# Performance work log

Measured on AMD Instinct MI355X. Metric: run time of the kernel, lower is better.

## Reference

```python
import jax, jax.numpy as jnp
import numpy as np

G, L, NSTA, NSRC, K = 10000, 1000, 400, 2000, 15
SIG = 10.0
FTRNS_SCALE = 1000.0  # ftrns1_diff(x) = x * 1000 (km -> m style linear transform)
FUDGE = 1.0


def setup_inputs() -> dict:
    key = jax.random.key(0)
    ks = jax.random.split(key, 9)
    sta = 10.0 * jax.random.normal(ks[0], (NSTA, 3), jnp.float32)
    src = 10.0 * jax.random.normal(ks[1], (NSRC, 3), jnp.float32)
    mag = jax.random.normal(ks[2], (NSRC,), jnp.float32)
    phase = jax.random.randint(ks[3], (NSTA,), 0, 2)
    x_grid = 10.0 * jax.random.normal(ks[4], (G, 3), jnp.float32)
    locs_ref = 10.0 * jax.random.normal(ks[5], (L, 3), jnp.float32)
    mag_coef = jnp.ones(2, jnp.float32)
    epicenter_spatial_coef = jnp.ones(2, jnp.float32)
    depth_spatial_coef = 0.1 * jax.random.normal(ks[6], (2,), jnp.float32)
    coefs = 0.1 * jax.random.normal(ks[7], (G, L, 2), jnp.float32)
    coefs_ker = SIG + 0.1 * jax.random.normal(ks[8], (G, L, 3), jnp.float32)
    return {"sta": sta, "src": src, "mag": mag, "phase": phase,
            "x_grid": x_grid, "locs_ref": locs_ref, "mag_coef": mag_coef,
            "epicenter_spatial_coef": epicenter_spatial_coef,
            "depth_spatial_coef": depth_spatial_coef,
            "coefs": coefs, "coefs_ker": coefs_ker}


def _ftrns(x):
    return x * FTRNS_SCALE


def _magnitude_fwd(sta, src, mag, phase, x_grid, locs_ref, mag_coef,
                   epicenter_spatial_coef, depth_spatial_coef, coefs, coefs_ker):
    sp = jax.nn.softplus
    zvec = jnp.array([1.0, 1.0, 0.0], dtype=sta.dtype)

    # nearest reference station index for each station (knn k=1)
    locs_ref_cart = _ftrns(locs_ref) / 1000.0            # [L,3]
    sta_pos = _ftrns(sta) / 1000.0                       # [Nsta,3]
    d2_ref = ((sta_pos[:, None, :] - locs_ref_cart[None, :, :]) ** 2).sum(-1)
    sta_ind = jnp.argmin(d2_ref, axis=1)                 # [Nsta]

    # pairwise log-distance matrices [Nsrc, Nsta]
    pw_log_dist_zero = jnp.log10(
        jnp.linalg.norm(_ftrns(src * zvec)[:, None, :] - _ftrns(sta * zvec)[None, :, :], axis=2) + FUDGE)
    pw_log_dist_depths = jnp.log10(jnp.abs(src[:, 2][:, None] - sta[:, 2][None, :]) + FUDGE)

    # --- anisotropic kNN interpolation of coefs[:, sta_ind, :] from grid to src ---
    pos1 = _ftrns(x_grid) / 1000.0                       # [G,3]
    pos2 = _ftrns(src) / 1000.0                          # [Nsrc,3]
    dq = ((pos2[:, None, :] - pos1[None, :, :]) ** 2).sum(-1)  # [Nsrc,G]
    _, idx = jax.lax.top_k(-dq, K)                       # [Nsrc,K] nearest grid nodes

    coefs_sub = coefs[:, sta_ind, :]                     # [G,Nsta,2]
    ker_sub = coefs_ker[:, sta_ind, :]                   # [G,Nsta,3]

    diff = pos1[idx] - pos2[:, None, :]                  # [Nsrc,K,3]
    ker_e = sp(ker_sub[idx])                             # [Nsrc,K,Nsta,3]
    w = jnp.exp(-0.5 * ((diff[:, :, None, :] / ker_e) ** 2).sum(-1))  # [Nsrc,K,Nsta]
    wsum = w.sum(axis=1, keepdims=True)                  # [Nsrc,1,Nsta]
    wsum = jnp.where(wsum == 0.0, 1.0, wsum)
    w = w / wsum
    bias_l = jnp.einsum('qkn,qknc->qnc', w, coefs_sub[idx])  # [Nsrc,Nsta,2]

    # phase-selected bias and coefficients
    bias = jnp.where(phase[None, :] == 0, bias_l[:, :, 0], bias_l[:, :, 1])  # [Nsrc,Nsta]
    mc = sp(mag_coef)[phase]                             # [Nsta]
    ec = sp(epicenter_spatial_coef)[phase]
    dc = depth_spatial_coef[phase]

    log_amp = (mag[:, None] * mc[None, :]
               - ec[None, :] * pw_log_dist_zero
               + dc[None, :] * pw_log_dist_depths
               + bias)                                   # [Nsrc,Nsta]
    return log_amp


def reference(sta, src, mag, phase, x_grid, locs_ref, mag_coef,
              epicenter_spatial_coef, depth_spatial_coef, coefs, coefs_ker):
    return _magnitude_fwd(sta, src, mag, phase, x_grid, locs_ref, mag_coef,
                          epicenter_spatial_coef, depth_spatial_coef, coefs, coefs_ker)
```

## Files before the change

kernel.cpp:

```cpp
#include <hip/hip_runtime.h>
#include <hip/hip_fp16.h>
#include <cstddef>

#define G_N   10000
#define L_N   1000
#define NSTA  400
#define NSRC  2000
#define KK    15
#define NBIN  2048
#define CAP   512

__device__ __forceinline__ float tr1k(float x) {
    return (x * 1000.0f) / 1000.0f;
}

__device__ __forceinline__ float softplus(float x) {
    return fmaxf(x, 0.0f) + log1pf(expf(-fabsf(x)));
}

__device__ __forceinline__ float softplus_fast(float x) {
    return fmaxf(x, 0.0f) + __logf(1.0f + __expf(-fabsf(x)));
}

__device__ __forceinline__ bool lexless(float v1, int i1, float v2, int i2) {
    return (v1 < v2) || (v1 == v2 && i1 < i2);
}

__global__ void sta_ind_kernel(const float* __restrict__ sta,
                               const float* __restrict__ locs_ref,
                               int* __restrict__ sta_ind,
                               int* __restrict__ used) {
#pragma clang fp contract(off)
    const int i    = blockIdx.x;
    const int lane = threadIdx.x;

    if (used) {
        int z = blockIdx.x * 64 + lane;
        if (z < G_N) used[z] = 0;
    }

    const float sx = tr1k(sta[i * 3 + 0]);
    const float sy = tr1k(sta[i * 3 + 1]);
    const float sz = tr1k(sta[i * 3 + 2]);
    float best = INFINITY;
    int   bidx = 0x7fffffff;
    for (int j = lane; j < L_N; j += 64) {
        float dx = sx - tr1k(locs_ref[j * 3 + 0]);
        float dy = sy - tr1k(locs_ref[j * 3 + 1]);
        float dz = sz - tr1k(locs_ref[j * 3 + 2]);
        float d  = (dx * dx + dy * dy) + dz * dz;
        if (lexless(d, j, best, bidx)) { best = d; bidx = j; }
    }
    for (int off = 1; off < 64; off <<= 1) {
        float ov = __shfl_xor(best, off);
        int   oi = __shfl_xor(bidx, off);
        if (lexless(ov, oi, best, bidx)) { best = ov; bidx = oi; }
    }
    if (lane == 0) sta_ind[i] = bidx;
}

__global__ __launch_bounds__(256, 8) void topk_kernel(const float* __restrict__ src,
                                                      const float* __restrict__ x_grid,
                                                      int* __restrict__ idx_out,
                                                      int* __restrict__ used) {
#pragma clang fp contract(off)
    const int s    = blockIdx.x;
    const int tid  = threadIdx.x;
    const int lane = tid & 63;
    const int wv   = tid >> 6;

    __shared__ unsigned int s_hist[NBIN];
    __shared__ int          s_cand[CAP];
    __shared__ float        s_cd[CAP];
    __shared__ int          s_cnt;
    __shared__ int          s_binB;
    __shared__ int          s_nle;
    __shared__ float        s_mv[4];
    __shared__ int          s_mi[4];
    __shared__ int          s_ch[KK];

    for (int b = tid; b < NBIN; b += 256) s_hist[b] = 0u;
    if (tid == 0) s_cnt = 0;
    __syncthreads();

    const float sx = tr1k(src[s * 3 + 0]);
    const float sy = tr1k(src[s * 3 + 1]);
    const float sz = tr1k(src[s * 3 + 2]);

    for (int g = tid; g < G_N; g += 256) {
        float dx = sx - tr1k(x_grid[g * 3 + 0]);
        float dy = sy - tr1k(x_grid[g * 3 + 1]);
        float dz = sz - tr1k(x_grid[g * 3 + 2]);
        float d  = (dx * dx + dy * dy) + dz * dz;
        atomicAdd(&s_hist[__float_as_uint(d) >> 20], 1u);
    }
    __syncthreads();

    if (wv == 0) {
        const int chunk = NBIN / 64;
        const int base  = lane * chunk;
        unsigned int cs = 0;
        for (int b = 0; b < chunk; ++b) cs += s_hist[base + b];
        unsigned int pfx = cs;
        for (int off = 1; off < 64; off <<= 1) {
            unsigned int o = __shfl_up(pfx, off);
            if (lane >= off) pfx += o;
        }
        unsigned long long m = __ballot(pfx >= (unsigned)KK);
        int fl = __ffsll((unsigned long long)m) - 1;
        if (lane == fl) {
            unsigned int acc = pfx - cs;
            int b = base;
            for (;;) {
                acc += s_hist[b];
                if (acc >= (unsigned)KK) break;
                ++b;
            }
            s_binB = b;
            s_nle  = (int)acc;
        }
    }
    __syncthreads();

    const int binB = s_binB;
    const int nle  = s_nle;

    if (nle <= CAP) {
        for (int g = tid; g < G_N; g += 256) {
            float dx = sx - tr1k(x_grid[g * 3 + 0]);
            float dy = sy - tr1k(x_grid[g * 3 + 1]);
            float dz = sz - tr1k(x_grid[g * 3 + 2]);
            float d  = (dx * dx + dy * dy) + dz * dz;
            if ((int)(__float_as_uint(d) >> 20) <= binB) {
                int p = atomicAdd(&s_cnt, 1);
                s_cand[p] = g;
                s_cd[p]   = d;
            }
        }
        __syncthreads();
        if (wv == 0) {
            const int n = s_cnt;
            float vals[KK];
            int   ids[KK];
#pragma unroll
            for (int j = 0; j < KK; ++j) { vals[j] = INFINITY; ids[j] = 0x7fffffff; }
            for (int c = lane; c < n; c += 64) {
                int   g = s_cand[c];
                float d = s_cd[c];
                if (lexless(d, g, vals[KK - 1], ids[KK - 1])) {
                    float cv = d; int ci = g;
#pragma unroll
                    for (int j = 0; j < KK; ++j) {
                        bool sw = lexless(cv, ci, vals[j], ids[j]);
                        float tv = sw ? vals[j] : cv;
                        int   ti = sw ? ids[j]  : ci;
                        vals[j]  = sw ? cv : vals[j];
                        ids[j]   = sw ? ci : ids[j];
                        cv = tv; ci = ti;
                    }
                }
            }
            for (int r = 0; r < KK; ++r) {
                float v  = vals[0];
                int   id = ids[0];
                int   who = lane;
                for (int off = 1; off < 64; off <<= 1) {
                    float ov = __shfl_xor(v, off);
                    int   oi = __shfl_xor(id, off);
                    int   ow = __shfl_xor(who, off);
                    if (lexless(ov, oi, v, id)) { v = ov; id = oi; who = ow; }
                }
                if (lane == 0) {
                    idx_out[s * KK + r] = id;
                    if (used) used[id] = 1;
                }
                if (who == lane) {
#pragma unroll
                    for (int j = 0; j < KK - 1; ++j) { vals[j] = vals[j + 1]; ids[j] = ids[j + 1]; }
                    vals[KK - 1] = INFINITY;
                    ids[KK - 1]  = 0x7fffffff;
                }
            }
        }
    } else {
        for (int r = 0; r < KK; ++r) {
            float v  = INFINITY;
            int   id = 0x7fffffff;
            for (int g = tid; g < G_N; g += 256) {
                bool skip = false;
                for (int j = 0; j < r; ++j) skip = skip || (s_ch[j] == g);
                if (skip) continue;
                float dx = sx - tr1k(x_grid[g * 3 + 0]);
                float dy = sy - tr1k(x_grid[g * 3 + 1]);
                float dz = sz - tr1k(x_grid[g * 3 + 2]);
                float d  = (dx * dx + dy * dy) + dz * dz;
                if (lexless(d, g, v, id)) { v = d; id = g; }
            }
            for (int off = 1; off < 64; off <<= 1) {
                float ov = __shfl_xor(v, off);
                int   oi = __shfl_xor(id, off);
                if (lexless(ov, oi, v, id)) { v = ov; id = oi; }
            }
            if (lane == 0) { s_mv[wv] = v; s_mi[wv] = id; }
            __syncthreads();
            if (tid == 0) {
                float bv = s_mv[0]; int bi = s_mi[0];
                for (int w = 1; w < 4; ++w)
                    if (lexless(s_mv[w], s_mi[w], bv, bi)) { bv = s_mv[w]; bi = s_mi[w]; }
                s_ch[r] = bi;
                idx_out[s * KK + r] = bi;
                if (used) used[bi] = 1;
            }
            __syncthreads();
        }
    }
}

__global__ __launch_bounds__(256) void pack_kernel(
    const float* __restrict__ coefs, const float* __restrict__ coefs_ker,
    const int* __restrict__ sta_ind, const int* __restrict__ phase,
    const int* __restrict__ used,
    uint2* __restrict__ pk)
{
    const int g = blockIdx.x;
    if (!used[g]) return;
    const int tid = threadIdx.x;

    __shared__ float s_ker[L_N * 3];
    __shared__ float s_c[L_N * 2];

    const float4* kr4 = (const float4*)(coefs_ker + (size_t)g * (L_N * 3));
    const float4* cr4 = (const float4*)(coefs     + (size_t)g * (L_N * 2));
    float4* sk4 = (float4*)s_ker;
    float4* sc4 = (float4*)s_c;
#pragma unroll
    for (int j = 0; j < 3; ++j) {
        int p = tid + j * 256;
        if (p < (L_N * 3) / 4) sk4[p] = kr4[p];
    }
#pragma unroll
    for (int j = 0; j < 2; ++j) {
        int p = tid + j * 256;
        if (p < (L_N * 2) / 4) sc4[p] = cr4[p];
    }
    const int i1 = tid + 256;
    const int st0 = sta_ind[tid];
    const int ph0 = phase[tid];
    const int st1 = (i1 < NSTA) ? sta_ind[i1] : 0;
    const int ph1 = (i1 < NSTA) ? phase[i1] : 0;
    __syncthreads();

    {
        float rk0 = 1.0f / softplus_fast(s_ker[st0 * 3 + 0]);
        float rk1 = 1.0f / softplus_fast(s_ker[st0 * 3 + 1]);
        float rk2 = 1.0f / softplus_fast(s_ker[st0 * 3 + 2]);
        float c   = (ph0 == 0) ? s_c[st0 * 2 + 0] : s_c[st0 * 2 + 1];
        __half2 a = __floats2half2_rn(rk0, rk1);
        __half2 b = __floats2half2_rn(rk2, c);
        uint2 u;
        u.x = *reinterpret_cast<unsigned int*>(&a);
        u.y = *reinterpret_cast<unsigned int*>(&b);
        pk[(size_t)g * NSTA + tid] = u;
    }
    if (i1 < NSTA) {
        float rk0 = 1.0f / softplus_fast(s_ker[st1 * 3 + 0]);
        float rk1 = 1.0f / softplus_fast(s_ker[st1 * 3 + 1]);
        float rk2 = 1.0f / softplus_fast(s_ker[st1 * 3 + 2]);
        float c   = (ph1 == 0) ? s_c[st1 * 2 + 0] : s_c[st1 * 2 + 1];
        __half2 a = __floats2half2_rn(rk0, rk1);
        __half2 b = __floats2half2_rn(rk2, c);
        uint2 u;
        u.x = *reinterpret_cast<unsigned int*>(&a);
        u.y = *reinterpret_cast<unsigned int*>(&b);
        pk[(size_t)g * NSTA + i1] = u;
    }
}

__global__ __launch_bounds__(256) void magnitude_fast_kernel(
    const float* __restrict__ sta, const float* __restrict__ src,
    const float* __restrict__ mag, const int* __restrict__ phase,
    const float* __restrict__ x_grid,
    const float* __restrict__ mag_coef, const float* __restrict__ epi_coef,
    const float* __restrict__ dep_coef,
    const uint2* __restrict__ pk, const int* __restrict__ idx,
    float* __restrict__ out)
{
    const int s   = blockIdx.x;
    const int tid = threadIdx.x;

    __shared__ float s_diff[KK][3];
    __shared__ int   s_g[KK];

    if (tid < KK) {
        int g = idx[s * KK + tid];
        s_g[tid] = g;
        s_diff[tid][0] = tr1k(x_grid[g * 3 + 0]) - tr1k(src[s * 3 + 0]);
        s_diff[tid][1] = tr1k(x_grid[g * 3 + 1]) - tr1k(src[s * 3 + 1]);
        s_diff[tid][2] = tr1k(x_grid[g * 3 + 2]) - tr1k(src[s * 3 + 2]);
    }
    __syncthreads();

    const float mag_s = mag[s];
    const float srcx = src[s * 3 + 0];
    const float srcy = src[s * 3 + 1];
    const float srcz = src[s * 3 + 2];
    const float sp_mc0 = softplus(mag_coef[0]), sp_mc1 = softplus(mag_coef[1]);
    const float sp_ec0 = softplus(epi_coef[0]), sp_ec1 = softplus(epi_coef[1]);
    const float dc0 = dep_coef[0], dc1 = dep_coef[1];

    for (int i = tid; i < NSTA; i += 256) {
        float wsum = 0.0f, a = 0.0f;
#pragma unroll
        for (int k = 0; k < KK; ++k) {
            uint2 u = pk[(size_t)s_g[k] * NSTA + i];
            __half2 h01 = *reinterpret_cast<const __half2*>(&u.x);
            __half2 h23 = *reinterpret_cast<const __half2*>(&u.y);
            float2 f01 = __half22float2(h01);
            float2 f23 = __half22float2(h23);
            float t0 = s_diff[k][0] * f01.x;
            float t1 = s_diff[k][1] * f01.y;
            float t2 = s_diff[k][2] * f23.x;
            float e  = __expf(-0.5f * ((t0 * t0 + t1 * t1) + t2 * t2));
            wsum += e;
            a    += e * f23.y;
        }
        if (wsum == 0.0f) wsum = 1.0f;

        const int ph = phase[i];
        float bias = a / wsum;

        float dx = srcx * 1000.0f - sta[i * 3 + 0] * 1000.0f;
        float dy = srcy * 1000.0f - sta[i * 3 + 1] * 1000.0f;
        float lz = __log10f(__fsqrt_rn(dx * dx + dy * dy) + 1.0f);
        float ld = __log10f(fabsf(srcz - sta[i * 3 + 2]) + 1.0f);

        float mc = (ph == 0) ? sp_mc0 : sp_mc1;
        float ec = (ph == 0) ? sp_ec0 : sp_ec1;
        float dc = (ph == 0) ? dc0 : dc1;

        out[(size_t)s * NSTA + i] = mag_s * mc - ec * lz + dc * ld + bias;
    }
}

__global__ __launch_bounds__(256) void magnitude_kernel(
    const float* __restrict__ sta, const float* __restrict__ src,
    const float* __restrict__ mag, const int* __restrict__ phase,
    const float* __restrict__ x_grid,
    const float* __restrict__ mag_coef, const float* __restrict__ epi_coef,
    const float* __restrict__ dep_coef,
    const float* __restrict__ coefs, const float* __restrict__ coefs_ker,
    const int* __restrict__ sta_ind, const int* __restrict__ idx,
    float* __restrict__ out)
{
    const int s   = blockIdx.x;
    const int tid = threadIdx.x;

    __shared__ float s_diff[KK][3];
    __shared__ int   s_g[KK];
    __shared__ int   s_sta[NSTA];

    if (tid < KK) {
        int g = idx[s * KK + tid];
        s_g[tid] = g;
        s_diff[tid][0] = tr1k(x_grid[g * 3 + 0]) - tr1k(src[s * 3 + 0]);
        s_diff[tid][1] = tr1k(x_grid[g * 3 + 1]) - tr1k(src[s * 3 + 1]);
        s_diff[tid][2] = tr1k(x_grid[g * 3 + 2]) - tr1k(src[s * 3 + 2]);
    }
    for (int i = tid; i < NSTA; i += 256) s_sta[i] = sta_ind[i];
    __syncthreads();

    const float mag_s = mag[s];
    const float srcx = src[s * 3 + 0];
    const float srcy = src[s * 3 + 1];
    const float srcz = src[s * 3 + 2];
    const float sp_mc0 = softplus(mag_coef[0]), sp_mc1 = softplus(mag_coef[1]);
    const float sp_ec0 = softplus(epi_coef[0]), sp_ec1 = softplus(epi_coef[1]);
    const float dc0 = dep_coef[0], dc1 = dep_coef[1];

    for (int i = tid; i < NSTA; i += 256) {
        const int st = s_sta[i];
        float wsum = 0.0f, a0 = 0.0f, a1 = 0.0f;
#pragma unroll
        for (int k = 0; k < KK; ++k) {
            const int g = s_g[k];
            const float* kp = coefs_ker + ((size_t)g * L_N + st) * 3;
            float k0 = softplus(kp[0]);
            float k1 = softplus(kp[1]);
            float k2 = softplus(kp[2]);
            float t0 = s_diff[k][0] / k0;
            float t1 = s_diff[k][1] / k1;
            float t2 = s_diff[k][2] / k2;
            float e  = expf(-0.5f * ((t0 * t0 + t1 * t1) + t2 * t2));
            const float* cp = coefs + ((size_t)g * L_N + st) * 2;
            wsum += e;
            a0 += e * cp[0];
            a1 += e * cp[1];
        }
        if (wsum == 0.0f) wsum = 1.0f;

        const int ph = phase[i];
        float bias = ((ph == 0) ? a0 : a1) / wsum;

        float dx = srcx * 1000.0f - sta[i * 3 + 0] * 1000.0f;
        float dy = srcy * 1000.0f - sta[i * 3 + 1] * 1000.0f;
        float lz = log10f(sqrtf(dx * dx + dy * dy) + 1.0f);
        float ld = log10f(fabsf(srcz - sta[i * 3 + 2]) + 1.0f);

        float mc = (ph == 0) ? sp_mc0 : sp_mc1;
        float ec = (ph == 0) ? sp_ec0 : sp_ec1;
        float dc = (ph == 0) ? dc0 : dc1;

        out[(size_t)s * NSTA + i] = mag_s * mc - ec * lz + dc * ld + bias;
    }
}

extern "C" void kernel_launch(void* const* d_in, const int* in_sizes, int n_in,
                              void* d_out, int out_size, void* d_ws, size_t ws_size,
                              hipStream_t stream) {
    const float* sta       = (const float*)d_in[0];
    const float* src       = (const float*)d_in[1];
    const float* mag       = (const float*)d_in[2];
    const int*   phase     = (const int*)d_in[3];
    const float* x_grid    = (const float*)d_in[4];
    const float* locs_ref  = (const float*)d_in[5];
    const float* mag_coef  = (const float*)d_in[6];
    const float* epi_coef  = (const float*)d_in[7];
    const float* dep_coef  = (const float*)d_in[8];
    const float* coefs     = (const float*)d_in[9];
    const float* coefs_ker = (const float*)d_in[10];
    float* out = (float*)d_out;

    const size_t pk_bytes = (size_t)G_N * NSTA * sizeof(uint2);
    const size_t need_fast = pk_bytes
                           + (size_t)NSRC * KK * sizeof(int)
                           + (size_t)NSTA * sizeof(int)
                           + (size_t)G_N * sizeof(int);

    if (ws_size >= need_fast) {
        uint2* ws_pk   = (uint2*)d_ws;
        int* ws_idx    = (int*)((char*)d_ws + pk_bytes);
        int* ws_sta    = ws_idx + (size_t)NSRC * KK;
        int* ws_used   = ws_sta + NSTA;

        hipLaunchKernelGGL(sta_ind_kernel, dim3(NSTA), dim3(64), 0, stream,
                           sta, locs_ref, ws_sta, ws_used);
        hipLaunchKernelGGL(topk_kernel, dim3(NSRC), dim3(256), 0, stream,
                           src, x_grid, ws_idx, ws_used);
        hipLaunchKernelGGL(pack_kernel, dim3(G_N), dim3(256), 0, stream,
                           coefs, coefs_ker, ws_sta, phase, ws_used, ws_pk);
        hipLaunchKernelGGL(magnitude_fast_kernel, dim3(NSRC), dim3(256), 0, stream,
                           sta, src, mag, phase, x_grid,
                           mag_coef, epi_coef, dep_coef,
                           ws_pk, ws_idx, out);
    } else {
        int* ws_sta = (int*)d_ws;
        int* ws_idx = ws_sta + NSTA;

        hipLaunchKernelGGL(sta_ind_kernel, dim3(NSTA), dim3(64), 0, stream,
                           sta, locs_ref, ws_sta, (int*)nullptr);
        hipLaunchKernelGGL(topk_kernel, dim3(NSRC), dim3(256), 0, stream,
                           src, x_grid, ws_idx, (int*)nullptr);
        hipLaunchKernelGGL(magnitude_kernel, dim3(NSRC), dim3(256), 0, stream,
                           sta, src, mag, phase, x_grid,
                           mag_coef, epi_coef, dep_coef,
                           coefs, coefs_ker, ws_sta, ws_idx, out);
    }
}
```

Baseline: 138.4 us.

## Fuse top-k and packing into one kernel and use min-based candidate threshold

Merges the top-k neighbour search and the coefficient packing into a single launch that interleaves one top-k block with five pack blocks, and packs every grid point instead of only those marked as used. The histogram pre-pass is replaced by a threshold taken from the 15th smallest of the per-thread minima, and transformed grid and source coordinates are precomputed once in the station prep kernel. This removes a launch and the histogram atomics and lets the two stages overlap. In exchange the pack stage now does work for all grid points, which adds memory traffic.

```diff
diff --git a/kernel.cpp b/kernel.cpp
--- a/kernel.cpp
+++ b/kernel.cpp
@@ -7,8 +7,9 @@
 #define NSTA  400
 #define NSRC  2000
 #define KK    15
-#define NBIN  2048
-#define CAP   512
+#define CAP   2048
+#define LDSB  20480
+#define CTLO  (1024 + 8 * CAP)
 
 __device__ __forceinline__ float tr1k(float x) {
     return (x * 1000.0f) / 1000.0f;
@@ -26,17 +27,21 @@
     return (v1 < v2) || (v1 == v2 && i1 < i2);
 }
 
-__global__ void sta_ind_kernel(const float* __restrict__ sta,
-                               const float* __restrict__ locs_ref,
-                               int* __restrict__ sta_ind,
-                               int* __restrict__ used) {
+__global__ void sta_prep_kernel(const float* __restrict__ sta,
+                                const float* __restrict__ locs_ref,
+                                const float* __restrict__ x_grid,
+                                const float* __restrict__ src,
+                                int* __restrict__ sta_ind,
+                                float* __restrict__ tg,
+                                float* __restrict__ ts) {
 #pragma clang fp contract(off)
     const int i    = blockIdx.x;
     const int lane = threadIdx.x;
 
-    if (used) {
-        int z = blockIdx.x * 64 + lane;
-        if (z < G_N) used[z] = 0;
+    const int z = i * 64 + lane;
+    for (int p = z; p < 3 * (G_N + NSRC); p += 400 * 64) {
+        if (p < 3 * G_N) tg[p] = tr1k(x_grid[p]);
+        else             ts[p - 3 * G_N] = tr1k(src[p - 3 * G_N]);
     }
 
     const float sx = tr1k(sta[i * 3 + 0]);
@@ -59,87 +64,86 @@
     if (lane == 0) sta_ind[i] = bidx;
 }
 
-__global__ __launch_bounds__(256, 8) void topk_kernel(const float* __restrict__ src,
-                                                      const float* __restrict__ x_grid,
-                                                      int* __restrict__ idx_out,
-                                                      int* __restrict__ used) {
+__device__ __forceinline__ void topk_block(int s,
+                                           const float* __restrict__ tg,
+                                           const float* __restrict__ ts,
+                                           int* __restrict__ idx_out,
+                                           char* s_raw, int tid) {
 #pragma clang fp contract(off)
-    const int s    = blockIdx.x;
-    const int tid  = threadIdx.x;
     const int lane = tid & 63;
     const int wv   = tid >> 6;
 
-    __shared__ unsigned int s_hist[NBIN];
-    __shared__ int          s_cand[CAP];
-    __shared__ float        s_cd[CAP];
-    __shared__ int          s_cnt;
-    __shared__ int          s_binB;
-    __shared__ int          s_nle;
-    __shared__ float        s_mv[4];
-    __shared__ int          s_mi[4];
-    __shared__ int          s_ch[KK];
-
-    for (int b = tid; b < NBIN; b += 256) s_hist[b] = 0u;
-    if (tid == 0) s_cnt = 0;
-    __syncthreads();
-
-    const float sx = tr1k(src[s * 3 + 0]);
-    const float sy = tr1k(src[s * 3 + 1]);
-    const float sz = tr1k(src[s * 3 + 2]);
-
+    float* s_min  = (float*)s_raw;
+    int*   s_cand = (int*)(s_raw + 1024);
+    float* s_cd   = (float*)(s_raw + 1024 + 4 * CAP);
+    float* s_T    = (float*)(s_raw + CTLO);
+    int*   s_cnt  = (int*)(s_raw + CTLO + 4);
+    float* s_mv   = (float*)(s_raw + CTLO + 8);
+    int*   s_mi   = (int*)(s_raw + CTLO + 24);
+    int*   s_ch   = (int*)(s_raw + CTLO + 40);
+
+    if (tid == 0) *s_cnt = 0;
+
+    const float sx = ts[s * 3 + 0];
+    const float sy = ts[s * 3 + 1];
+    const float sz = ts[s * 3 + 2];
+
+    float mymin = INFINITY;
     for (int g = tid; g < G_N; g += 256) {
-        float dx = sx - tr1k(x_grid[g * 3 + 0]);
-        float dy = sy - tr1k(x_grid[g * 3 + 1]);
-        float dz = sz - tr1k(x_grid[g * 3 + 2]);
+        float dx = sx - tg[g * 3 + 0];
+        float dy = sy - tg[g * 3 + 1];
+        float dz = sz - tg[g * 3 + 2];
         float d  = (dx * dx + dy * dy) + dz * dz;
-        atomicAdd(&s_hist[__float_as_uint(d) >> 20], 1u);
-    }
+        mymin = fminf(mymin, d);
+    }
+    s_min[tid] = mymin;
     __syncthreads();
 
     if (wv == 0) {
-        const int chunk = NBIN / 64;
-        const int base  = lane * chunk;
-        unsigned int cs = 0;
-        for (int b = 0; b < chunk; ++b) cs += s_hist[base + b];
-        unsigned int pfx = cs;
-        for (int off = 1; off < 64; off <<= 1) {
-            unsigned int o = __shfl_up(pfx, off);
-            if (lane >= off) pfx += o;
-        }
-        unsigned long long m = __ballot(pfx >= (unsigned)KK);
-        int fl = __ffsll((unsigned long long)m) - 1;
-        if (lane == fl) {
-            unsigned int acc = pfx - cs;
-            int b = base;
-            for (;;) {
-                acc += s_hist[b];
-                if (acc >= (unsigned)KK) break;
-                ++b;
-            }
-            s_binB = b;
-            s_nle  = (int)acc;
-        }
-    }
-    __syncthreads();
-
-    const int binB = s_binB;
-    const int nle  = s_nle;
-
-    if (nle <= CAP) {
-        for (int g = tid; g < G_N; g += 256) {
-            float dx = sx - tr1k(x_grid[g * 3 + 0]);
-            float dy = sy - tr1k(x_grid[g * 3 + 1]);
-            float dz = sz - tr1k(x_grid[g * 3 + 2]);
-            float d  = (dx * dx + dy * dy) + dz * dz;
-            if ((int)(__float_as_uint(d) >> 20) <= binB) {
-                int p = atomicAdd(&s_cnt, 1);
-                s_cand[p] = g;
-                s_cd[p]   = d;
-            }
-        }
-        __syncthreads();
+        float m0 = s_min[lane];
+        float m1 = s_min[lane + 64];
+        float m2 = s_min[lane + 128];
+        float m3 = s_min[lane + 192];
+        float T = INFINITY;
+        for (int r = 0; r < KK; ++r) {
+            float lv = m0; int ls = 0;
+            if (m1 < lv) { lv = m1; ls = 1; }
+            if (m2 < lv) { lv = m2; ls = 2; }
+            if (m3 < lv) { lv = m3; ls = 3; }
+            float v = lv; int wl = lane;
+            for (int off = 1; off < 64; off <<= 1) {
+                float ov = __shfl_xor(v, off);
+                int   ol = __shfl_xor(wl, off);
+                if (ov < v || (ov == v && ol < wl)) { v = ov; wl = ol; }
+            }
+            T = v;
+            if (wl == lane) {
+                if (ls == 0) m0 = INFINITY;
+                else if (ls == 1) m1 = INFINITY;
+                else if (ls == 2) m2 = INFINITY;
+                else m3 = INFINITY;
+            }
+        }
+        if (lane == 0) *s_T = T;
+    }
+    __syncthreads();
+    const float T = *s_T;
+
+    for (int g = tid; g < G_N; g += 256) {
+        float dx = sx - tg[g * 3 + 0];
+        float dy = sy - tg[g * 3 + 1];
+        float dz = sz - tg[g * 3 + 2];
+        float d  = (dx * dx + dy * dy) + dz * dz;
+        if (d <= T) {
+            int p = atomicAdd(s_cnt, 1);
+            if (p < CAP) { s_cand[p] = g; s_cd[p] = d; }
+        }
+    }
+    __syncthreads();
+    const int n = *s_cnt;
+
+    if (n <= CAP) {
         if (wv == 0) {
-            const int n = s_cnt;
             float vals[KK];
             int   ids[KK];
 #pragma unroll
@@ -170,10 +174,7 @@
                     int   ow = __shfl_xor(who, off);
                     if (lexless(ov, oi, v, id)) { v = ov; id = oi; who = ow; }
                 }
-                if (lane == 0) {
-                    idx_out[s * KK + r] = id;
-                    if (used) used[id] = 1;
-                }
+                if (lane == 0) idx_out[s * KK + r] = id;
                 if (who == lane) {
 #pragma unroll
                     for (int j = 0; j < KK - 1; ++j) { vals[j] = vals[j + 1]; ids[j] = ids[j + 1]; }
@@ -190,9 +191,9 @@
                 bool skip = false;
                 for (int j = 0; j < r; ++j) skip = skip || (s_ch[j] == g);
                 if (skip) continue;
-                float dx = sx - tr1k(x_grid[g * 3 + 0]);
-                float dy = sy - tr1k(x_grid[g * 3 + 1]);
-                float dz = sz - tr1k(x_grid[g * 3 + 2]);
+                float dx = sx - tg[g * 3 + 0];
+                float dy = sy - tg[g * 3 + 1];
+                float dz = sz - tg[g * 3 + 2];
                 float d  = (dx * dx + dy * dy) + dz * dz;
                 if (lexless(d, g, v, id)) { v = d; id = g; }
             }
@@ -209,25 +210,21 @@
                     if (lexless(s_mv[w], s_mi[w], bv, bi)) { bv = s_mv[w]; bi = s_mi[w]; }
                 s_ch[r] = bi;
                 idx_out[s * KK + r] = bi;
-                if (used) used[bi] = 1;
             }
             __syncthreads();
         }
     }
 }
 
-__global__ __launch_bounds__(256) void pack_kernel(
-    const float* __restrict__ coefs, const float* __restrict__ coefs_ker,
-    const int* __restrict__ sta_ind, const int* __restrict__ phase,
-    const int* __restrict__ used,
-    uint2* __restrict__ pk)
-{
-    const int g = blockIdx.x;
-    if (!used[g]) return;
-    const int tid = threadIdx.x;
-
-    __shared__ float s_ker[L_N * 3];
-    __shared__ float s_c[L_N * 2];
+__device__ __forceinline__ void pack_block(int g,
+                                           const float* __restrict__ coefs,
+                                           const float* __restrict__ coefs_ker,
+                                           const int* __restrict__ sta_ind,
+                                           const int* __restrict__ phase,
+                                           uint2* __restrict__ pk,
+                                           char* s_raw, int tid) {
+    float* s_ker = (float*)s_raw;
+    float* s_c   = (float*)(s_raw + 12288);
 
     const float4* kr4 = (const float4*)(coefs_ker + (size_t)g * (L_N * 3));
     const float4* cr4 = (const float4*)(coefs     + (size_t)g * (L_N * 2));
@@ -243,7 +240,7 @@
         int p = tid + j * 256;
         if (p < (L_N * 2) / 4) sc4[p] = cr4[p];
     }
-    const int i1 = tid + 256;
+    const int i1  = tid + 256;
     const int st0 = sta_ind[tid];
     const int ph0 = phase[tid];
     const int st1 = (i1 < NSTA) ? sta_ind[i1] : 0;
@@ -274,6 +271,31 @@
         u.y = *reinterpret_cast<unsigned int*>(&b);
         pk[(size_t)g * NSTA + i1] = u;
     }
+}
+
+__global__ __launch_bounds__(256, 8) void fused_kernel(
+    const float* __restrict__ coefs, const float* __restrict__ coefs_ker,
+    const int* __restrict__ sta_ind, const int* __restrict__ phase,
+    uint2* __restrict__ pk,
+    const float* __restrict__ tg, const float* __restrict__ ts,
+    int* __restrict__ idx_out)
+{
+    __shared__ __align__(16) char s_raw[LDSB];
+    const int bid = blockIdx.x;
+    const int t = bid / 6, r = bid % 6;
+    if (r == 5) {
+        topk_block(t, tg, ts, idx_out, s_raw, threadIdx.x);
+    } else {
+        pack_block(t * 5 + r, coefs, coefs_ker, sta_ind, phase, pk, s_raw, threadIdx.x);
+    }
+}
+
+__global__ __launch_bounds__(256, 8) void topk_only_kernel(
+    const float* __restrict__ tg, const float* __restrict__ ts,
+    int* __restrict__ idx_out)
+{
+    __shared__ __align__(16) char s_raw[LDSB];
+    topk_block(blockIdx.x, tg, ts, idx_out, s_raw, threadIdx.x);
 }
 
 __global__ __launch_bounds__(256) void magnitude_fast_kernel(
@@ -431,35 +453,35 @@
     float* out = (float*)d_out;
 
     const size_t pk_bytes = (size_t)G_N * NSTA * sizeof(uint2);
-    const size_t need_fast = pk_bytes
-                           + (size_t)NSRC * KK * sizeof(int)
-                           + (size_t)NSTA * sizeof(int)
-                           + (size_t)G_N * sizeof(int);
+    const size_t tail_ints = (size_t)NSRC * KK + NSTA + 3 * G_N + 3 * NSRC;
+    const size_t need_fast = pk_bytes + tail_ints * 4;
 
     if (ws_size >= need_fast) {
         uint2* ws_pk   = (uint2*)d_ws;
-        int* ws_idx    = (int*)((char*)d_ws + pk_bytes);
-        int* ws_sta    = ws_idx + (size_t)NSRC * KK;
-        int* ws_used   = ws_sta + NSTA;
-
-        hipLaunchKernelGGL(sta_ind_kernel, dim3(NSTA), dim3(64), 0, stream,
-                           sta, locs_ref, ws_sta, ws_used);
-        hipLaunchKernelGGL(topk_kernel, dim3(NSRC), dim3(256), 0, stream,
-                           src, x_grid, ws_idx, ws_used);
-        hipLaunchKernelGGL(pack_kernel, dim3(G_N), dim3(256), 0, stream,
-                           coefs, coefs_ker, ws_sta, phase, ws_used, ws_pk);
+        int*   ws_idx  = (int*)((char*)d_ws + pk_bytes);
+        int*   ws_sta  = ws_idx + (size_t)NSRC * KK;
+        float* ws_tg   = (float*)(ws_sta + NSTA);
+        float* ws_ts   = ws_tg + 3 * G_N;
+
+        hipLaunchKernelGGL(sta_prep_kernel, dim3(NSTA), dim3(64), 0, stream,
+                           sta, locs_ref, x_grid, src, ws_sta, ws_tg, ws_ts);
+        hipLaunchKernelGGL(fused_kernel, dim3(6 * NSRC), dim3(256), 0, stream,
+                           coefs, coefs_ker, ws_sta, phase, ws_pk,
+                           ws_tg, ws_ts, ws_idx);
         hipLaunchKernelGGL(magnitude_fast_kernel, dim3(NSRC), dim3(256), 0, stream,
                            sta, src, mag, phase, x_grid,
                            mag_coef, epi_coef, dep_coef,
                            ws_pk, ws_idx, out);
     } else {
-        int* ws_sta = (int*)d_ws;
-        int* ws_idx = ws_sta + NSTA;
-
-        hipLaunchKernelGGL(sta_ind_kernel, dim3(NSTA), dim3(64), 0, stream,
-                           sta, locs_ref, ws_sta, (int*)nullptr);
-        hipLaunchKernelGGL(topk_kernel, dim3(NSRC), dim3(256), 0, stream,
-                           src, x_grid, ws_idx, (int*)nullptr);
+        int*   ws_sta = (int*)d_ws;
+        int*   ws_idx = ws_sta + NSTA;
+        float* ws_tg  = (float*)(ws_idx + (size_t)NSRC * KK);
+        float* ws_ts  = ws_tg + 3 * G_N;
+
+        hipLaunchKernelGGL(sta_prep_kernel, dim3(NSTA), dim3(64), 0, stream,
+                           sta, locs_ref, x_grid, src, ws_sta, ws_tg, ws_ts);
+        hipLaunchKernelGGL(topk_only_kernel, dim3(NSRC), dim3(256), 0, stream,
+                           ws_tg, ws_ts, ws_idx);
         hipLaunchKernelGGL(magnitude_kernel, dim3(NSRC), dim3(256), 0, stream,
                            sta, src, mag, phase, x_grid,
                            mag_coef, epi_coef, dep_coef,
```

Result: no change. 136.6 us (-1.3%).
